# Optimization experiments

Measured on AMD Instinct MI355X. Metric: run time of the kernel, lower is better.

## Reference

```python
import jax, jax.numpy as jnp
import numpy as np

D_MODEL = 1024
HIDDEN = 4096
N_EXPERTS = 8
TOP_K = 2


def setup_inputs() -> dict:
    key = jax.random.key(0)
    k_x, k_r, k_w1, k_w2 = jax.random.split(key, 4)
    x = jax.random.normal(k_x, (2, 1024, D_MODEL), dtype=jnp.float32)
    # router: nn.Linear(d_model, n_experts, bias=False) -> weight [E, D]; store transposed [D, E]
    Wr = jax.random.normal(k_r, (D_MODEL, N_EXPERTS), dtype=jnp.float32) * 0.02
    # expert w1: Linear(D, H) -> store [E, D, H]; w2: Linear(H, D) -> [E, H, D]
    W1 = jax.random.normal(k_w1, (N_EXPERTS, D_MODEL, HIDDEN), dtype=jnp.float32) * 0.02
    W2 = jax.random.normal(k_w2, (N_EXPERTS, HIDDEN, D_MODEL), dtype=jnp.float32) * 0.02
    return {"x": x, "Wr": Wr, "W1": W1, "W2": W2}


def reference(x, Wr, W1, W2):
    B, S, D = x.shape
    flat = x.reshape(-1, D)                       # [T, D]
    logits = flat @ Wr                            # [T, E]
    top_vals, top_idx = jax.lax.top_k(logits, TOP_K)
    # softmax over the top-k logits; forward only uses slot 0 (faithful to source)
    weights = jax.nn.softmax(top_vals, axis=-1)   # [T, K]
    top1 = top_idx[:, 0]                          # [T] int
    w_top1 = weights[:, 0]                        # [T]
    # dense all-expert compute (fixed small E loop fused into batched einsum)
    h = jax.nn.gelu(jnp.einsum('td,edh->teh', flat, W1), approximate=False)  # [T,E,H]
    y = jnp.einsum('teh,ehd->ted', h, W2)         # [T, E, D]
    y_sel = jnp.take_along_axis(y, top1[:, None, None], axis=1)[:, 0, :]     # [T, D]
    out = (w_top1[:, None] * y_sel).reshape(B, S, D)
    return out
```

## Files before the change

kernel.cpp:

```cpp
#include <hip/hip_runtime.h>
#include <hip/hip_bf16.h>
#include <math.h>

#define T_TOKENS 2048
#define DMODEL   1024
#define HID      4096
#define NEXP     8
#define MAX_TILES 64

typedef float  f32x4  __attribute__((ext_vector_type(4)));
typedef short  bf16x8 __attribute__((ext_vector_type(8)));
typedef unsigned short u16x8 __attribute__((ext_vector_type(8)));

__device__ __forceinline__ unsigned short f2bf(float f) {
    union { float f; unsigned u; } v; v.f = f;
    unsigned u = v.u;
    unsigned r = (u + 0x7FFFu + ((u >> 16) & 1u)) >> 16;
    return (unsigned short)r;
}

__device__ __forceinline__ void async_copy16(const void* g, void* l) {
    __builtin_amdgcn_global_load_lds(
        (const __attribute__((address_space(1))) void*)g,
        (__attribute__((address_space(3))) void*)l,
        16, 0, 0);
}

__device__ __forceinline__ float gelu_f(float v) {
    float z = fabsf(v) * 0.70710678118654752f;
    float t = 1.f / (1.f + 0.3275911f * z);
    float poly = t * (0.254829592f + t * (-0.284496736f + t * (1.421413741f
               + t * (-1.453152027f + t * 1.061405429f))));
    float erfv = 1.f - poly * __expf(-z * z);
    erfv = copysignf(erfv, v);
    return 0.5f * v * (1.f + erfv);
}

__global__ void router_kernel(const float* __restrict__ x, const float* __restrict__ Wr,
                              int* counts, int* expert_of, int* slot_of, float* wt_of) {
    int t = blockIdx.x;
    int lane = threadIdx.x;
    const float* xr = x + (size_t)t * DMODEL;
    float p[NEXP];
#pragma unroll
    for (int e = 0; e < NEXP; ++e) p[e] = 0.f;
    for (int d = lane; d < DMODEL; d += 64) {
        float xv = xr[d];
        const float* wr = Wr + (size_t)d * NEXP;
#pragma unroll
        for (int e = 0; e < NEXP; ++e) p[e] += xv * wr[e];
    }
#pragma unroll
    for (int e = 0; e < NEXP; ++e) {
        for (int off = 32; off > 0; off >>= 1)
            p[e] += __shfl_down(p[e], off, 64);
    }
    if (lane == 0) {
        int i0 = 0; float v0 = p[0];
        for (int e = 1; e < NEXP; ++e) if (p[e] > v0) { v0 = p[e]; i0 = e; }
        float v1 = -INFINITY;
        for (int e = 0; e < NEXP; ++e) if (e != i0 && p[e] > v1) v1 = p[e];
        float w = 1.f / (1.f + expf(v1 - v0));
        expert_of[t] = i0;
        wt_of[t] = w;
        slot_of[t] = atomicAdd(&counts[i0], 1);
    }
}

__global__ void scan_scatter_kernel(const int* counts, const int* expert_of,
                                    const int* slot_of, int* offsets, int* perm,
                                    int* tileE, int* tileM, int* tileCount) {
    __shared__ int offs[NEXP];
    if (threadIdx.x == 0) {
        int run = 0, tc = 0;
        for (int e = 0; e < NEXP; ++e) {
            offsets[e] = run; offs[e] = run;
            for (int m0 = 0; m0 < counts[e]; m0 += 64) { tileE[tc] = e; tileM[tc] = m0; ++tc; }
            run += counts[e];
        }
        *tileCount = tc;
    }
    __syncthreads();
    for (int t = threadIdx.x; t < T_TOKENS; t += 256)
        perm[offs[expert_of[t]] + slot_of[t]] = t;
}

__global__ __launch_bounds__(256) void convert_transpose_kernel(
    const float* __restrict__ W, unsigned short* __restrict__ WT, int K, int N) {
    int ktiles = K >> 6, ntiles = N >> 6;
    int gid = blockIdx.x;
    int e   = gid / (ktiles * ntiles);
    int r   = gid % (ktiles * ntiles);
    int kt  = r / ntiles, nt = r % ntiles;
    const float* src = W + (size_t)e * K * N + (size_t)(kt * 64) * N + nt * 64;
    unsigned short* dst = WT + (size_t)e * N * K + (size_t)(nt * 64) * K + kt * 64;

    __shared__ unsigned short tile[64][66];
    int tid = threadIdx.x;
    int n4 = (tid & 15) * 4;
    int kk = tid >> 4;
#pragma unroll
    for (int p = 0; p < 4; ++p) {
        int k = kk + p * 16;
        float4 v = *(const float4*)(src + (size_t)k * N + n4);
        tile[n4 + 0][k] = f2bf(v.x);
        tile[n4 + 1][k] = f2bf(v.y);
        tile[n4 + 2][k] = f2bf(v.z);
        tile[n4 + 3][k] = f2bf(v.w);
    }
    __syncthreads();
    int n = tid >> 2, ks = (tid & 3) * 16;
    unsigned short tmp[16];
#pragma unroll
    for (int i = 0; i < 16; ++i) tmp[i] = tile[n][ks + i];
    *(u16x8*)(dst + (size_t)n * K + ks)     = *(u16x8*)&tmp[0];
    *(u16x8*)(dst + (size_t)n * K + ks + 8) = *(u16x8*)&tmp[8];
}

__global__ __launch_bounds__(256) void convert_x_kernel(
    const float* __restrict__ x, unsigned short* __restrict__ xbf) {
    int i = (blockIdx.x * 256 + threadIdx.x) * 4;
    float4 v = *(const float4*)(x + i);
    ushort4 b;
    b.x = f2bf(v.x); b.y = f2bf(v.y); b.z = f2bf(v.z); b.w = f2bf(v.w);
    *(ushort4*)(xbf + i) = b;
}

__global__ __launch_bounds__(256, 4) void gemm1_kernel(
    const unsigned short* __restrict__ Xbf, const unsigned short* __restrict__ W1T,
    const int* __restrict__ counts, const int* __restrict__ offsets,
    const int* __restrict__ perm, const int* __restrict__ tileE,
    const int* __restrict__ tileM, const int* __restrict__ tileCount,
    unsigned short* __restrict__ H) {

    const int NT = HID / 128;
    int tile = blockIdx.x / NT;
    int nt   = blockIdx.x % NT;
    if (tile >= *tileCount) return;
    int e = tileE[tile], m0 = tileM[tile];
    int rows_e = counts[e], base = offsets[e];
    int n0 = nt * 128;

    __shared__ unsigned short Alds[64 * 64];
    __shared__ unsigned short Blds[128 * 64];

    int tid  = threadIdx.x;
    int lane = tid & 63;
    int wid  = tid >> 6;
    int wm = wid >> 1, wn = wid & 1;

    const unsigned short* ag[2]; unsigned short* al[2];
    const unsigned short* bg[4]; unsigned short* bl[4];
#pragma unroll
    for (int p = 0; p < 2; ++p) {
        int idx = p * 256 + tid;
        int row = idx >> 3, seg = idx & 7;
        int r = m0 + row;
        int tok = perm[base + (r < rows_e ? r : rows_e - 1)];
        ag[p] = Xbf + (size_t)tok * DMODEL + seg * 8;
        al[p] = &Alds[idx * 8];
    }
#pragma unroll
    for (int p = 0; p < 4; ++p) {
        int idx = p * 256 + tid;
        int row = idx >> 3, seg = idx & 7;
        bg[p] = W1T + ((size_t)e * HID + n0 + row) * DMODEL + seg * 8;
        bl[p] = &Blds[idx * 8];
    }

    f32x4 acc[2][4];
#pragma unroll
    for (int i = 0; i < 2; ++i)
#pragma unroll
        for (int j = 0; j < 4; ++j) acc[i][j] = (f32x4){0.f, 0.f, 0.f, 0.f};

    for (int k0 = 0; k0 < DMODEL; k0 += 64) {
        __syncthreads();
#pragma unroll
        for (int p = 0; p < 2; ++p) async_copy16(ag[p] + k0, al[p]);
#pragma unroll
        for (int p = 0; p < 4; ++p) async_copy16(bg[p] + k0, bl[p]);
        __syncthreads();
#pragma unroll
        for (int ks = 0; ks < 2; ++ks) {
            int kq = ks * 32 + (lane >> 4) * 8;
            bf16x8 af[2], bfr[4];
#pragma unroll
            for (int i = 0; i < 2; ++i) {
                int m = wm * 32 + i * 16 + (lane & 15);
                af[i] = *(const bf16x8*)&Alds[m * 64 + kq];
            }
#pragma unroll
            for (int j = 0; j < 4; ++j) {
                int n = wn * 64 + j * 16 + (lane & 15);
                bfr[j] = *(const bf16x8*)&Blds[n * 64 + kq];
            }
#pragma unroll
            for (int i = 0; i < 2; ++i)
#pragma unroll
                for (int j = 0; j < 4; ++j)
                    acc[i][j] = __builtin_amdgcn_mfma_f32_16x16x32_bf16(af[i], bfr[j], acc[i][j], 0, 0, 0);
        }
    }

    int quad = lane >> 4, col = lane & 15;
#pragma unroll
    for (int i = 0; i < 2; ++i)
#pragma unroll
        for (int j = 0; j < 4; ++j)
#pragma unroll
            for (int r = 0; r < 4; ++r) {
                int ml = wm * 32 + i * 16 + quad * 4 + r;
                if (m0 + ml < rows_e) {
                    int n = n0 + wn * 64 + j * 16 + col;
                    H[(size_t)(base + m0 + ml) * HID + n] = f2bf(gelu_f(acc[i][j][r]));
                }
            }
}

__global__ __launch_bounds__(256, 4) void gemm2_kernel(
    const unsigned short* __restrict__ H, const unsigned short* __restrict__ W2T,
    const int* __restrict__ counts, const int* __restrict__ offsets,
    const int* __restrict__ perm, const float* __restrict__ wt_of,
    const int* __restrict__ tileE, const int* __restrict__ tileM,
    const int* __restrict__ tileCount, float* __restrict__ part) {

    const int NT = DMODEL / 128;
    int tile = blockIdx.x / (NT * 2);
    int rem  = blockIdx.x % (NT * 2);
    int nt   = rem >> 1;
    int sk   = rem & 1;
    if (tile >= *tileCount) return;
    int e = tileE[tile], m0 = tileM[tile];
    int rows_e = counts[e], base = offsets[e];
    int n0 = nt * 128;
    int kbeg = sk * (HID / 2), kend = kbeg + (HID / 2);

    __shared__ unsigned short Alds[64 * 64];
    __shared__ unsigned short Blds[128 * 64];
    __shared__ float rowW[64];

    int tid  = threadIdx.x;
    int lane = tid & 63;
    int wid  = tid >> 6;
    int wm = wid >> 1, wn = wid & 1;

    if (tid < 64) {
        int r = m0 + tid;
        rowW[tid] = (r < rows_e) ? wt_of[perm[base + r]] : 0.f;
    }

    const unsigned short* ag[2]; unsigned short* al[2];
    const unsigned short* bg[4]; unsigned short* bl[4];
#pragma unroll
    for (int p = 0; p < 2; ++p) {
        int idx = p * 256 + tid;
        int row = idx >> 3, seg = idx & 7;
        int hr = base + m0 + row;
        if (hr > T_TOKENS - 1) hr = T_TOKENS - 1;
        ag[p] = H + (size_t)hr * HID + seg * 8;
        al[p] = &Alds[idx * 8];
    }
#pragma unroll
    for (int p = 0; p < 4; ++p) {
        int idx = p * 256 + tid;
        int row = idx >> 3, seg = idx & 7;
        bg[p] = W2T + ((size_t)e * DMODEL + n0 + row) * HID + seg * 8;
        bl[p] = &Blds[idx * 8];
    }

    f32x4 acc[2][4];
#pragma unroll
    for (int i = 0; i < 2; ++i)
#pragma unroll
        for (int j = 0; j < 4; ++j) acc[i][j] = (f32x4){0.f, 0.f, 0.f, 0.f};

    for (int k0 = kbeg; k0 < kend; k0 += 64) {
        __syncthreads();
#pragma unroll
        for (int p = 0; p < 2; ++p) async_copy16(ag[p] + k0, al[p]);
#pragma unroll
        for (int p = 0; p < 4; ++p) async_copy16(bg[p] + k0, bl[p]);
        __syncthreads();
#pragma unroll
        for (int ks = 0; ks < 2; ++ks) {
            int kq = ks * 32 + (lane >> 4) * 8;
            bf16x8 af[2], bfr[4];
#pragma unroll
            for (int i = 0; i < 2; ++i) {
                int m = wm * 32 + i * 16 + (lane & 15);
                af[i] = *(const bf16x8*)&Alds[m * 64 + kq];
            }
#pragma unroll
            for (int j = 0; j < 4; ++j) {
                int n = wn * 64 + j * 16 + (lane & 15);
                bfr[j] = *(const bf16x8*)&Blds[n * 64 + kq];
            }
#pragma unroll
            for (int i = 0; i < 2; ++i)
#pragma unroll
                for (int j = 0; j < 4; ++j)
                    acc[i][j] = __builtin_amdgcn_mfma_f32_16x16x32_bf16(af[i], bfr[j], acc[i][j], 0, 0, 0);
        }
    }

    float* dst = part + (size_t)sk * T_TOKENS * DMODEL;
    int quad = lane >> 4, col = lane & 15;
#pragma unroll
    for (int i = 0; i < 2; ++i)
#pragma unroll
        for (int j = 0; j < 4; ++j)
#pragma unroll
            for (int r = 0; r < 4; ++r) {
                int ml = wm * 32 + i * 16 + quad * 4 + r;
                if (m0 + ml < rows_e) {
                    int n = n0 + wn * 64 + j * 16 + col;
                    dst[(size_t)(base + m0 + ml) * DMODEL + n] = rowW[ml] * acc[i][j][r];
                }
            }
}

__global__ __launch_bounds__(256) void reduce_kernel(
    const float* __restrict__ part, const int* __restrict__ perm,
    float* __restrict__ out) {
    int row = blockIdx.x;
    int tok = perm[row];
    const float4* p0 = (const float4*)(part + (size_t)row * DMODEL);
    const float4* p1 = (const float4*)(part + (size_t)(T_TOKENS + row) * DMODEL);
    float4* o = (float4*)(out + (size_t)tok * DMODEL);
    int c = threadIdx.x;
    float4 a = p0[c], b = p1[c];
    o[c] = make_float4(a.x + b.x, a.y + b.y, a.z + b.z, a.w + b.w);
}

extern "C" void kernel_launch(void* const* d_in, const int* in_sizes, int n_in,
                              void* d_out, int out_size, void* d_ws, size_t ws_size,
                              hipStream_t stream) {
    const float* x  = (const float*)d_in[0];
    const float* Wr = (const float*)d_in[1];
    const float* W1 = (const float*)d_in[2];
    const float* W2 = (const float*)d_in[3];
    float* out = (float*)d_out;

    char* ws = (char*)d_ws;
    int*   counts    = (int*)(ws);
    int*   offsets   = (int*)(ws + 64);
    int*   tileCount = (int*)(ws + 128);
    int*   tileE     = (int*)(ws + 256);
    int*   tileM     = (int*)(ws + 256 + 4 * MAX_TILES);
    int*   expert_of = (int*)(ws + 1024);
    int*   slot_of   = (int*)(ws + 1024 + 8192);
    float* wt_of     = (float*)(ws + 1024 + 16384);
    int*   perm      = (int*)(ws + 1024 + 24576);
    size_t off = 65536;
    unsigned short* Xbf  = (unsigned short*)(ws + off); off += (size_t)T_TOKENS * DMODEL * 2;
    unsigned short* Hbuf = (unsigned short*)(ws + off); off += (size_t)T_TOKENS * HID * 2;
    float*          Part = (float*)(ws + off);          off += (size_t)2 * T_TOKENS * DMODEL * 4;
    unsigned short* W1T  = (unsigned short*)(ws + off); off += (size_t)NEXP * DMODEL * HID * 2;
    unsigned short* W2T  = (unsigned short*)(ws + off);

    hipMemsetAsync(counts, 0, 64, stream);
    router_kernel<<<T_TOKENS, 64, 0, stream>>>(x, Wr, counts, expert_of, slot_of, wt_of);
    scan_scatter_kernel<<<1, 256, 0, stream>>>(counts, expert_of, slot_of,
                                               offsets, perm, tileE, tileM, tileCount);
    convert_x_kernel<<<(T_TOKENS * DMODEL) / 1024, 256, 0, stream>>>(x, Xbf);
    convert_transpose_kernel<<<NEXP * (DMODEL / 64) * (HID / 64), 256, 0, stream>>>(W1, W1T, DMODEL, HID);
    gemm1_kernel<<<MAX_TILES * (HID / 128), 256, 0, stream>>>(
        Xbf, W1T, counts, offsets, perm, tileE, tileM, tileCount, Hbuf);
    convert_transpose_kernel<<<NEXP * (HID / 64) * (DMODEL / 64), 256, 0, stream>>>(W2, W2T, HID, DMODEL);
    gemm2_kernel<<<MAX_TILES * (DMODEL / 128) * 2, 256, 0, stream>>>(
        Hbuf, W2T, counts, offsets, perm, wt_of, tileE, tileM, tileCount, Part);
    reduce_kernel<<<T_TOKENS, 256, 0, stream>>>(Part, perm, out);
}
```

Baseline: 444.7 us.

## Fuse x conversion into router, merge weight converts, drop split-K reduce

The router kernel now also converts x to bf16 with vectorized float4 loads, so the separate convert_x kernel goes away. The scan kernel counts experts and builds perm itself using shared-memory atomics, which removes the memset and the slot_of array. Both weight transposes now run in a single launch. gemm2 drops split-K and writes weighted results straight into the output rows through the token permutation, which removes the partial buffer and the reduce kernel. The trade-off is that gemm2 launches half as many blocks, each with twice the K work, and MAX_TILES is cut to the true upper bound of 40 to avoid launching empty blocks.

```diff
diff --git a/kernel.cpp b/kernel.cpp
--- a/kernel.cpp
+++ b/kernel.cpp
@@ -6,7 +6,7 @@
 #define DMODEL   1024
 #define HID      4096
 #define NEXP     8
-#define MAX_TILES 64
+#define MAX_TILES 40
 
 typedef float  f32x4  __attribute__((ext_vector_type(4)));
 typedef short  bf16x8 __attribute__((ext_vector_type(8)));
@@ -36,19 +36,29 @@
     return 0.5f * v * (1.f + erfv);
 }
 
-__global__ void router_kernel(const float* __restrict__ x, const float* __restrict__ Wr,
-                              int* counts, int* expert_of, int* slot_of, float* wt_of) {
+__global__ __launch_bounds__(64) void router_kernel(
+    const float* __restrict__ x, const float* __restrict__ Wr,
+    int* __restrict__ expert_of, float* __restrict__ wt_of,
+    unsigned short* __restrict__ xbf) {
     int t = blockIdx.x;
     int lane = threadIdx.x;
     const float* xr = x + (size_t)t * DMODEL;
+    unsigned short* xb = xbf + (size_t)t * DMODEL;
     float p[NEXP];
 #pragma unroll
     for (int e = 0; e < NEXP; ++e) p[e] = 0.f;
-    for (int d = lane; d < DMODEL; d += 64) {
-        float xv = xr[d];
-        const float* wr = Wr + (size_t)d * NEXP;
-#pragma unroll
-        for (int e = 0; e < NEXP; ++e) p[e] += xv * wr[e];
+#pragma unroll
+    for (int q = 0; q < 4; ++q) {
+        int d = q * 256 + lane * 4;
+        float4 v = *(const float4*)(xr + d);
+        ushort4 b;
+        b.x = f2bf(v.x); b.y = f2bf(v.y); b.z = f2bf(v.z); b.w = f2bf(v.w);
+        *(ushort4*)(xb + d) = b;
+        const float* w0 = Wr + (size_t)d * NEXP;
+#pragma unroll
+        for (int e = 0; e < NEXP; ++e)
+            p[e] += v.x * w0[e] + v.y * w0[NEXP + e] + v.z * w0[2 * NEXP + e]
+                  + v.w * w0[3 * NEXP + e];
     }
 #pragma unroll
     for (int e = 0; e < NEXP; ++e) {
@@ -60,35 +70,48 @@
         for (int e = 1; e < NEXP; ++e) if (p[e] > v0) { v0 = p[e]; i0 = e; }
         float v1 = -INFINITY;
         for (int e = 0; e < NEXP; ++e) if (e != i0 && p[e] > v1) v1 = p[e];
-        float w = 1.f / (1.f + expf(v1 - v0));
         expert_of[t] = i0;
-        wt_of[t] = w;
-        slot_of[t] = atomicAdd(&counts[i0], 1);
-    }
-}
-
-__global__ void scan_scatter_kernel(const int* counts, const int* expert_of,
-                                    const int* slot_of, int* offsets, int* perm,
-                                    int* tileE, int* tileM, int* tileCount) {
-    __shared__ int offs[NEXP];
-    if (threadIdx.x == 0) {
+        wt_of[t] = 1.f / (1.f + expf(v1 - v0));
+    }
+}
+
+__global__ __launch_bounds__(256) void scan_scatter_kernel(
+    const int* __restrict__ expert_of, int* __restrict__ counts,
+    int* __restrict__ offsets, int* __restrict__ perm,
+    int* __restrict__ tileE, int* __restrict__ tileM, int* __restrict__ tileCount) {
+    __shared__ int cnt[NEXP];
+    __shared__ int off2[NEXP];
+    int tid = threadIdx.x;
+    if (tid < NEXP) cnt[tid] = 0;
+    __syncthreads();
+    for (int t = tid; t < T_TOKENS; t += 256)
+        atomicAdd(&cnt[expert_of[t]], 1);
+    __syncthreads();
+    if (tid == 0) {
         int run = 0, tc = 0;
         for (int e = 0; e < NEXP; ++e) {
-            offsets[e] = run; offs[e] = run;
-            for (int m0 = 0; m0 < counts[e]; m0 += 64) { tileE[tc] = e; tileM[tc] = m0; ++tc; }
-            run += counts[e];
+            counts[e] = cnt[e];
+            offsets[e] = run; off2[e] = run;
+            for (int m0 = 0; m0 < cnt[e]; m0 += 64) { tileE[tc] = e; tileM[tc] = m0; ++tc; }
+            run += cnt[e];
         }
         *tileCount = tc;
     }
     __syncthreads();
-    for (int t = threadIdx.x; t < T_TOKENS; t += 256)
-        perm[offs[expert_of[t]] + slot_of[t]] = t;
-}
-
-__global__ __launch_bounds__(256) void convert_transpose_kernel(
-    const float* __restrict__ W, unsigned short* __restrict__ WT, int K, int N) {
+    for (int t = tid; t < T_TOKENS; t += 256) {
+        int slot = atomicAdd(&off2[expert_of[t]], 1);
+        perm[slot] = t;
+    }
+}
+
+__global__ __launch_bounds__(256) void convert_w_kernel(
+    const float* __restrict__ W1, unsigned short* __restrict__ W1T,
+    const float* __restrict__ W2, unsigned short* __restrict__ W2T) {
+    int gid = blockIdx.x;
+    const float* W; unsigned short* WT; int K, N;
+    if (gid < 8192) { W = W1; WT = W1T; K = DMODEL; N = HID; }
+    else            { W = W2; WT = W2T; K = HID; N = DMODEL; gid -= 8192; }
     int ktiles = K >> 6, ntiles = N >> 6;
-    int gid = blockIdx.x;
     int e   = gid / (ktiles * ntiles);
     int r   = gid % (ktiles * ntiles);
     int kt  = r / ntiles, nt = r % ntiles;
@@ -117,15 +140,6 @@
     *(u16x8*)(dst + (size_t)n * K + ks + 8) = *(u16x8*)&tmp[8];
 }
 
-__global__ __launch_bounds__(256) void convert_x_kernel(
-    const float* __restrict__ x, unsigned short* __restrict__ xbf) {
-    int i = (blockIdx.x * 256 + threadIdx.x) * 4;
-    float4 v = *(const float4*)(x + i);
-    ushort4 b;
-    b.x = f2bf(v.x); b.y = f2bf(v.y); b.z = f2bf(v.z); b.w = f2bf(v.w);
-    *(ushort4*)(xbf + i) = b;
-}
-
 __global__ __launch_bounds__(256, 4) void gemm1_kernel(
     const unsigned short* __restrict__ Xbf, const unsigned short* __restrict__ W1T,
     const int* __restrict__ counts, const int* __restrict__ offsets,
@@ -223,21 +237,19 @@
     const int* __restrict__ counts, const int* __restrict__ offsets,
     const int* __restrict__ perm, const float* __restrict__ wt_of,
     const int* __restrict__ tileE, const int* __restrict__ tileM,
-    const int* __restrict__ tileCount, float* __restrict__ part) {
+    const int* __restrict__ tileCount, float* __restrict__ out) {
 
     const int NT = DMODEL / 128;
-    int tile = blockIdx.x / (NT * 2);
-    int rem  = blockIdx.x % (NT * 2);
-    int nt   = rem >> 1;
-    int sk   = rem & 1;
+    int tile = blockIdx.x / NT;
+    int nt   = blockIdx.x % NT;
     if (tile >= *tileCount) return;
     int e = tileE[tile], m0 = tileM[tile];
     int rows_e = counts[e], base = offsets[e];
     int n0 = nt * 128;
-    int kbeg = sk * (HID / 2), kend = kbeg + (HID / 2);
 
     __shared__ unsigned short Alds[64 * 64];
     __shared__ unsigned short Blds[128 * 64];
+    __shared__ int   rowTok[64];
     __shared__ float rowW[64];
 
     int tid  = threadIdx.x;
@@ -247,7 +259,11 @@
 
     if (tid < 64) {
         int r = m0 + tid;
-        rowW[tid] = (r < rows_e) ? wt_of[perm[base + r]] : 0.f;
+        if (r < rows_e) {
+            int tok = perm[base + r];
+            rowTok[tid] = tok;
+            rowW[tid]   = wt_of[tok];
+        } else { rowTok[tid] = 0; rowW[tid] = 0.f; }
     }
 
     const unsigned short* ag[2]; unsigned short* al[2];
@@ -275,7 +291,7 @@
 #pragma unroll
         for (int j = 0; j < 4; ++j) acc[i][j] = (f32x4){0.f, 0.f, 0.f, 0.f};
 
-    for (int k0 = kbeg; k0 < kend; k0 += 64) {
+    for (int k0 = 0; k0 < HID; k0 += 64) {
         __syncthreads();
 #pragma unroll
         for (int p = 0; p < 2; ++p) async_copy16(ag[p] + k0, al[p]);
@@ -304,7 +320,6 @@
         }
     }
 
-    float* dst = part + (size_t)sk * T_TOKENS * DMODEL;
     int quad = lane >> 4, col = lane & 15;
 #pragma unroll
     for (int i = 0; i < 2; ++i)
@@ -314,23 +329,11 @@
             for (int r = 0; r < 4; ++r) {
                 int ml = wm * 32 + i * 16 + quad * 4 + r;
                 if (m0 + ml < rows_e) {
+                    int tok = rowTok[ml];
                     int n = n0 + wn * 64 + j * 16 + col;
-                    dst[(size_t)(base + m0 + ml) * DMODEL + n] = rowW[ml] * acc[i][j][r];
+                    out[(size_t)tok * DMODEL + n] = rowW[ml] * acc[i][j][r];
                 }
             }
-}
-
-__global__ __launch_bounds__(256) void reduce_kernel(
-    const float* __restrict__ part, const int* __restrict__ perm,
-    float* __restrict__ out) {
-    int row = blockIdx.x;
-    int tok = perm[row];
-    const float4* p0 = (const float4*)(part + (size_t)row * DMODEL);
-    const float4* p1 = (const float4*)(part + (size_t)(T_TOKENS + row) * DMODEL);
-    float4* o = (float4*)(out + (size_t)tok * DMODEL);
-    int c = threadIdx.x;
-    float4 a = p0[c], b = p1[c];
-    o[c] = make_float4(a.x + b.x, a.y + b.y, a.z + b.z, a.w + b.w);
 }
 
 extern "C" void kernel_launch(void* const* d_in, const int* in_sizes, int n_in,
@@ -349,26 +352,20 @@
     int*   tileE     = (int*)(ws + 256);
     int*   tileM     = (int*)(ws + 256 + 4 * MAX_TILES);
     int*   expert_of = (int*)(ws + 1024);
-    int*   slot_of   = (int*)(ws + 1024 + 8192);
-    float* wt_of     = (float*)(ws + 1024 + 16384);
-    int*   perm      = (int*)(ws + 1024 + 24576);
+    float* wt_of     = (float*)(ws + 1024 + 8192);
+    int*   perm      = (int*)(ws + 1024 + 16384);
     size_t off = 65536;
     unsigned short* Xbf  = (unsigned short*)(ws + off); off += (size_t)T_TOKENS * DMODEL * 2;
     unsigned short* Hbuf = (unsigned short*)(ws + off); off += (size_t)T_TOKENS * HID * 2;
-    float*          Part = (float*)(ws + off);          off += (size_t)2 * T_TOKENS * DMODEL * 4;
     unsigned short* W1T  = (unsigned short*)(ws + off); off += (size_t)NEXP * DMODEL * HID * 2;
     unsigned short* W2T  = (unsigned short*)(ws + off);
 
-    hipMemsetAsync(counts, 0, 64, stream);
-    router_kernel<<<T_TOKENS, 64, 0, stream>>>(x, Wr, counts, expert_of, slot_of, wt_of);
-    scan_scatter_kernel<<<1, 256, 0, stream>>>(counts, expert_of, slot_of,
-                                               offsets, perm, tileE, tileM, tileCount);
-    convert_x_kernel<<<(T_TOKENS * DMODEL) / 1024, 256, 0, stream>>>(x, Xbf);
-    convert_transpose_kernel<<<NEXP * (DMODEL / 64) * (HID / 64), 256, 0, stream>>>(W1, W1T, DMODEL, HID);
+    router_kernel<<<T_TOKENS, 64, 0, stream>>>(x, Wr, expert_of, wt_of, Xbf);
+    scan_scatter_kernel<<<1, 256, 0, stream>>>(expert_of, counts, offsets, perm,
+                                               tileE, tileM, tileCount);
+    convert_w_kernel<<<16384, 256, 0, stream>>>(W1, W1T, W2, W2T);
     gemm1_kernel<<<MAX_TILES * (HID / 128), 256, 0, stream>>>(
         Xbf, W1T, counts, offsets, perm, tileE, tileM, tileCount, Hbuf);
-    convert_transpose_kernel<<<NEXP * (HID / 64) * (DMODEL / 64), 256, 0, stream>>>(W2, W2T, HID, DMODEL);
-    gemm2_kernel<<<MAX_TILES * (DMODEL / 128) * 2, 256, 0, stream>>>(
-        Hbuf, W2T, counts, offsets, perm, wt_of, tileE, tileM, tileCount, Part);
-    reduce_kernel<<<T_TOKENS, 256, 0, stream>>>(Part, perm, out);
-}
+    gemm2_kernel<<<MAX_TILES * (DMODEL / 128), 256, 0, stream>>>(
+        Hbuf, W2T, counts, offsets, perm, wt_of, tileE, tileM, tileCount, out);
+}
```

Measured after the change: 449.9 us. About the same (+1.2%).
